# Performance work log

Hardware: AMD Instinct MI355X
Metric: run time of the kernel (lower is better)

The kernel has to match this reference:

```python
import jax, jax.numpy as jnp
import numpy as np

BSZ, SEQ, HID = 8, 4096, 1024
N_EXPERTS = 8
CAPACITY = 512  # expert_capacity_per_batch; effective cap = min(SEQ, CAPACITY)
SCALE = 1.0     # routed_scaling_factor


def setup_inputs() -> dict:
    key = jax.random.key(0)
    k1, k2 = jax.random.split(key)
    hidden_states = jax.random.normal(k1, (BSZ, SEQ, HID), dtype=jnp.float32)
    # kaiming_uniform_(a=sqrt(5)) on [d,e] -> bound = 1/sqrt(fan_in=d)
    bound = 1.0 / np.sqrt(HID)
    weight = jax.random.uniform(k2, (HID, N_EXPERTS), dtype=jnp.float32,
                                minval=-bound, maxval=bound)
    return {"hidden_states": hidden_states, "weight": weight}


def reference(hidden_states, weight):
    bsz, seq_len, h = hidden_states.shape
    # gating logits in fp32: [b, s, e]
    logits = jnp.einsum('bsd,de->bse', hidden_states.astype(jnp.float32),
                        weight.astype(jnp.float32))
    affinity = jax.nn.softmax(logits, axis=-1)          # [b, s, e]
    affinity = jnp.transpose(affinity, (0, 2, 1))       # [b, e, s]
    cap = min(seq_len, CAPACITY)                        # static
    # Each expert picks its top-`cap` tokens (sorted descending, like torch.topk)
    topk_scores, topk_indices = jax.lax.top_k(affinity, cap)  # [b, e, cap]
    topk_scores = topk_scores * SCALE
    # dense dispatch mask [b, e, cap, s]: one-hot over token positions
    dispatch_mask = jax.nn.one_hot(topk_indices, seq_len, dtype=jnp.float32)
    return topk_indices, topk_scores, dispatch_mask
```

## Files before the change

kernel.cpp:

```cpp
#include <hip/hip_runtime.h>

constexpr int BSZ = 8, SEQ = 4096, HID = 1024, NE = 8, CAP = 512;
constexpr int ROWS = BSZ * NE;
constexpr size_t IDX_ELEMS = (size_t)ROWS * CAP;
constexpr size_t SCR_OFF = IDX_ELEMS;
constexpr size_t MASK_OFF = IDX_ELEMS * 2;
constexpr size_t MASK_ELEMS = (size_t)ROWS * CAP * SEQ;
constexpr size_t AFF_ELEMS = (size_t)ROWS * SEQ;

typedef float f4v __attribute__((ext_vector_type(4)));

__global__ __launch_bounds__(128) void gating_kernel(const float* __restrict__ hidden,
                                                     const float* __restrict__ weight,
                                                     float* __restrict__ aff)
{
    __shared__ float hls[16][68];
    __shared__ float wls[8][68];
    __shared__ float lls[16][8];

    const int tid = threadIdx.x;
    const int T0 = blockIdx.x * 16;
    const int t = tid >> 3;
    const int e = tid & 7;

    float v0 = 0.f, v1 = 0.f, v2 = 0.f, v3 = 0.f;
    for (int c = 0; c < 16; ++c) {
        __syncthreads();
#pragma unroll
        for (int k = 0; k < 2; ++k) {
            const int j = tid + k * 128;
            const int tt = j >> 4, q = j & 15;
            const float4 v = *(const float4*)(hidden + (size_t)(T0 + tt) * HID + c * 64 + 4 * q);
            *(float4*)&hls[tt][4 * q] = v;
        }
#pragma unroll
        for (int k = 0; k < 4; ++k) {
            const int j = tid + k * 128;
            const int dd = j >> 3, ee = j & 7;
            wls[ee][dd] = weight[(size_t)(c * 64 + dd) * NE + ee];
        }
        __syncthreads();
#pragma unroll
        for (int k = 0; k < 4; ++k) {
            const int base = 16 * k;
            const float4 hA = *(const float4*)&hls[t][base + 0];
            const float4 hB = *(const float4*)&hls[t][base + 4];
            const float4 hC = *(const float4*)&hls[t][base + 8];
            const float4 hD = *(const float4*)&hls[t][base + 12];
            const float4 wA = *(const float4*)&wls[e][base + 0];
            const float4 wB = *(const float4*)&wls[e][base + 4];
            const float4 wC = *(const float4*)&wls[e][base + 8];
            const float4 wD = *(const float4*)&wls[e][base + 12];
            v0 = __fadd_rn(__fmul_rn(hA.x, wA.x),
                 __fadd_rn(__fmul_rn(hB.x, wB.x),
                 __fadd_rn(__fmul_rn(hC.x, wC.x),
                 __fadd_rn(__fmul_rn(hD.x, wD.x), v0))));
            v1 = __fadd_rn(__fmul_rn(hA.y, wA.y),
                 __fadd_rn(__fmul_rn(hB.y, wB.y),
                 __fadd_rn(__fmul_rn(hC.y, wC.y),
                 __fadd_rn(__fmul_rn(hD.y, wD.y), v1))));
            v2 = __fadd_rn(__fmul_rn(hA.z, wA.z),
                 __fadd_rn(__fmul_rn(hB.z, wB.z),
                 __fadd_rn(__fmul_rn(hC.z, wC.z),
                 __fadd_rn(__fmul_rn(hD.z, wD.z), v2))));
            v3 = __fadd_rn(__fmul_rn(hA.w, wA.w),
                 __fadd_rn(__fmul_rn(hB.w, wB.w),
                 __fadd_rn(__fmul_rn(hC.w, wC.w),
                 __fadd_rn(__fmul_rn(hD.w, wD.w), v3))));
        }
    }
    const float logit = __fadd_rn(__fadd_rn(v0, v1), __fadd_rn(v2, v3));

    lls[t][e] = logit;
    __syncthreads();

    float l[8];
#pragma unroll
    for (int k = 0; k < 8; ++k) l[k] = lls[t][k];
    float m = l[0];
#pragma unroll
    for (int k = 1; k < 8; ++k) m = fmaxf(m, l[k]);
    float p[8];
#pragma unroll
    for (int k = 0; k < 8; ++k)
        p[k] = (float)exp((double)__fsub_rn(l[k], m));
    const float s = __fadd_rn(__fadd_rn(__fadd_rn(p[0], p[1]), __fadd_rn(p[2], p[3])),
                              __fadd_rn(__fadd_rn(p[4], p[5]), __fadd_rn(p[6], p[7])));
    const float a = __fdiv_rn(p[e], s);

    const int token = T0 + t;
    const int b = token >> 12;
    const int sidx = token & (SEQ - 1);
    aff[((size_t)b * NE + e) * SEQ + sidx] = a;
}

__global__ __launch_bounds__(1024) void sortzero_kernel(const float* __restrict__ aff,
                                                        float* __restrict__ out)
{
    __shared__ unsigned long long keys[SEQ];
    const int row = blockIdx.x;
    const float* a = aff + (size_t)row * SEQ;
    float* mrow = out + MASK_OFF + (size_t)row * CAP * SEQ;

    for (int i = threadIdx.x; i < SEQ; i += 1024) {
        const unsigned int fb = __float_as_uint(a[i]);
        keys[i] = ((unsigned long long)fb << 32) | (unsigned int)(SEQ - 1 - i);
    }

    f4v* mz = (f4v*)mrow;
    const f4v z4 = {0.f, 0.f, 0.f, 0.f};
    int zi = 0;

    for (int len = 2; len <= SEQ; len <<= 1) {
        for (int stride = len >> 1; stride > 0; stride >>= 1) {
            __syncthreads();
#pragma unroll
            for (int k = 0; k < 7; ++k) {
                if (zi < 512) {
                    __builtin_nontemporal_store(z4, mz + (size_t)zi * 1024 + threadIdx.x);
                    ++zi;
                }
            }
            for (int t = threadIdx.x; t < SEQ / 2; t += 1024) {
                const int i = (t << 1) - (t & (stride - 1));
                const int j = i + stride;
                const unsigned long long ki = keys[i], kj = keys[j];
                const bool desc = ((i & len) == 0);
                if (desc ? (ki < kj) : (ki > kj)) { keys[i] = kj; keys[j] = ki; }
            }
        }
    }
    __syncthreads();
    if (threadIdx.x < CAP) {
        const int t = threadIdx.x;
        const unsigned long long k = keys[t];
        const int idx = (SEQ - 1) - (int)(unsigned int)(k & 0xffffffffu);
        out[(size_t)row * CAP + t] = (float)idx;
        out[SCR_OFF + (size_t)row * CAP + t] =
            __uint_as_float((unsigned int)(k >> 32));
        mrow[(size_t)t * SEQ + idx] = 1.0f;
    }
}

__global__ __launch_bounds__(1024) void topk_zero_kernel(const float* __restrict__ aff,
                                                         float* __restrict__ out,
                                                         long long zero_elems)
{
    __shared__ unsigned long long keys[SEQ];
    if (blockIdx.x < (unsigned)ROWS) {
        const int row = blockIdx.x;
        const float* a = aff + (size_t)row * SEQ;
        for (int i = threadIdx.x; i < SEQ; i += 1024) {
            const unsigned int fb = __float_as_uint(a[i]);
            keys[i] = ((unsigned long long)fb << 32) | (unsigned int)(SEQ - 1 - i);
        }
        for (int len = 2; len <= SEQ; len <<= 1) {
            for (int stride = len >> 1; stride > 0; stride >>= 1) {
                __syncthreads();
                for (int t = threadIdx.x; t < SEQ / 2; t += 1024) {
                    const int i = (t << 1) - (t & (stride - 1));
                    const int j = i + stride;
                    const unsigned long long ki = keys[i], kj = keys[j];
                    const bool desc = ((i & len) == 0);
                    if (desc ? (ki < kj) : (ki > kj)) { keys[i] = kj; keys[j] = ki; }
                }
            }
        }
        __syncthreads();
        if (threadIdx.x < CAP) {
            const int t = threadIdx.x;
            const unsigned long long k = keys[t];
            const int idx = (SEQ - 1) - (int)(unsigned int)(k & 0xffffffffu);
            out[(size_t)row * CAP + t] = (float)idx;
            out[SCR_OFF + (size_t)row * CAP + t] =
                __uint_as_float((unsigned int)(k >> 32));
        }
    } else {
        const long long nz4 = zero_elems >> 2;
        f4v* mz = (f4v*)(out + MASK_OFF);
        const f4v z4 = {0.f, 0.f, 0.f, 0.f};
        const long long stride = (long long)(gridDim.x - ROWS) * 1024;
        for (long long i = (long long)(blockIdx.x - ROWS) * 1024 + threadIdx.x;
             i < nz4; i += stride)
            __builtin_nontemporal_store(z4, mz + i);
    }
}

__global__ void tailzero_kernel(float* __restrict__ out)
{
    const long long n4 = (long long)(AFF_ELEMS >> 2);
    f4v* mz = (f4v*)(out + MASK_OFF + MASK_ELEMS - AFF_ELEMS);
    const f4v z4 = {0.f, 0.f, 0.f, 0.f};
    const long long i = (long long)blockIdx.x * blockDim.x + threadIdx.x;
    if (i < n4) __builtin_nontemporal_store(z4, mz + i);
}

__global__ void scatter_kernel(float* __restrict__ out)
{
    const int p = blockIdx.x * blockDim.x + threadIdx.x;
    if (p < (int)IDX_ELEMS) {
        const int idx = (int)out[p];
        out[MASK_OFF + (size_t)p * SEQ + idx] = 1.0f;
    }
}

extern "C" void kernel_launch(void* const* d_in, const int* in_sizes, int n_in,
                              void* d_out, int out_size, void* d_ws, size_t ws_size,
                              hipStream_t stream)
{
    const float* hidden = (const float*)d_in[0];
    const float* weight = (const float*)d_in[1];
    float* out = (float*)d_out;

    const bool use_ws = (ws_size >= AFF_ELEMS * sizeof(float));

    if (use_ws) {
        float* aff = (float*)d_ws;
        gating_kernel<<<2048, 128, 0, stream>>>(hidden, weight, aff);
        sortzero_kernel<<<ROWS, 1024, 0, stream>>>(aff, out);
    } else {
        float* aff = out + MASK_OFF + MASK_ELEMS - AFF_ELEMS;
        gating_kernel<<<2048, 128, 0, stream>>>(hidden, weight, aff);
        const long long zero_elems = (long long)(MASK_ELEMS - AFF_ELEMS);
        topk_zero_kernel<<<ROWS + 1984, 1024, 0, stream>>>(aff, out, zero_elems);
        tailzero_kernel<<<256, 256, 0, stream>>>(out);
        scatter_kernel<<<(int)((IDX_ELEMS + 255) / 256), 256, 0, stream>>>(out);
    }
}
```

Measured before the change: 640.0 us.

## Split top-k into segmented bitonic sorts plus bitonic merge-selection kernel

Replaces the one-block-per-row full 4096-element bitonic sort with a two-stage scheme. Stage one sorts each 512-element segment in 512 blocks while 1536 other blocks zero the dispatch mask. Stage two merges the segments with bitonic top-half selection and writes indices, scores and one-hot entries. The aim is more parallelism and less wasted sorting work, since only the top 512 per row are needed. It costs an extra workspace buffer for the keys, an extra global round trip and an extra launch, and it needs a larger workspace or it falls back to the old path.

```diff
diff --git a/kernel.cpp b/kernel.cpp
--- a/kernel.cpp
+++ b/kernel.cpp
@@ -7,6 +7,8 @@
 constexpr size_t MASK_OFF = IDX_ELEMS * 2;
 constexpr size_t MASK_ELEMS = (size_t)ROWS * CAP * SEQ;
 constexpr size_t AFF_ELEMS = (size_t)ROWS * SEQ;
+constexpr size_t AFF_BYTES = AFF_ELEMS * sizeof(float);
+constexpr size_t KEYS_BYTES = (size_t)ROWS * SEQ * 8;
 
 typedef float f4v __attribute__((ext_vector_type(4)));
 
@@ -94,6 +96,86 @@
     aff[((size_t)b * NE + e) * SEQ + sidx] = a;
 }
 
+__global__ __launch_bounds__(256) void segsort_zero_kernel(const float* __restrict__ aff,
+                                                           unsigned long long* __restrict__ keys,
+                                                           float* __restrict__ out)
+{
+    __shared__ unsigned long long k[512];
+    if (blockIdx.x < 512) {
+        const int row = blockIdx.x >> 3, seg = blockIdx.x & 7;
+        const int g0 = seg * 512;
+        const float* a = aff + (size_t)row * SEQ + g0;
+        for (int j = threadIdx.x; j < 512; j += 256) {
+            const unsigned int fb = __float_as_uint(a[j]);
+            k[j] = ((unsigned long long)fb << 32) | (unsigned int)(SEQ - 1 - (g0 + j));
+        }
+        for (int len = 2; len <= 512; len <<= 1) {
+            for (int stride = len >> 1; stride > 0; stride >>= 1) {
+                __syncthreads();
+                const int t = threadIdx.x;
+                const int i = (t << 1) - (t & (stride - 1));
+                const int j = i + stride;
+                const unsigned long long ki = k[i], kj = k[j];
+                const bool desc = ((i & len) == 0);
+                if (desc ? (ki < kj) : (ki > kj)) { k[i] = kj; k[j] = ki; }
+            }
+        }
+        __syncthreads();
+        unsigned long long* dst = keys + (size_t)row * SEQ + g0;
+        for (int j = threadIdx.x; j < 512; j += 256) dst[j] = k[j];
+    } else {
+        const long long nz4 = (long long)(MASK_ELEMS >> 2);
+        f4v* mz = (f4v*)(out + MASK_OFF);
+        const f4v z4 = {0.f, 0.f, 0.f, 0.f};
+        const long long stride = (long long)(2048 - 512) * 256;
+        for (long long i = (long long)(blockIdx.x - 512) * 256 + threadIdx.x;
+             i < nz4; i += stride)
+            __builtin_nontemporal_store(z4, mz + i);
+    }
+}
+
+__global__ __launch_bounds__(512) void merge_scatter_kernel(const unsigned long long* __restrict__ keys,
+                                                            float* __restrict__ out)
+{
+    __shared__ unsigned long long A[SEQ];
+    const int row = blockIdx.x;
+    for (int i = threadIdx.x; i < SEQ; i += 512)
+        A[i] = keys[(size_t)row * SEQ + i];
+
+    for (int round = 0; round < 3; ++round) {
+        const int sp = 1024 << round;
+        const int npairs = 4 >> round;
+        __syncthreads();
+        for (int u = threadIdx.x; u < npairs * 512; u += 512) {
+            const int p = u >> 9, i = u & 511;
+            const int base = p * sp;
+            const unsigned long long x = A[base + i];
+            const unsigned long long y = A[base + sp / 2 + 511 - i];
+            if (y > x) A[base + i] = y;
+        }
+        for (int s = 256; s > 0; s >>= 1) {
+            __syncthreads();
+            for (int u = threadIdx.x; u < npairs * 256; u += 512) {
+                const int r = u >> 8, t2 = u & 255;
+                const int base = r * sp;
+                const int i = (t2 << 1) - (t2 & (s - 1));
+                const unsigned long long x = A[base + i], y = A[base + i + s];
+                if (y > x) { A[base + i] = y; A[base + i + s] = x; }
+            }
+        }
+    }
+    __syncthreads();
+    if (threadIdx.x < CAP) {
+        const int t = threadIdx.x;
+        const unsigned long long k = A[t];
+        const int idx = (SEQ - 1) - (int)(unsigned int)(k & 0xffffffffu);
+        out[(size_t)row * CAP + t] = (float)idx;
+        out[SCR_OFF + (size_t)row * CAP + t] =
+            __uint_as_float((unsigned int)(k >> 32));
+        out[MASK_OFF + ((size_t)row * CAP + t) * SEQ + idx] = 1.0f;
+    }
+}
+
 __global__ __launch_bounds__(1024) void sortzero_kernel(const float* __restrict__ aff,
                                                         float* __restrict__ out)
 {
@@ -106,11 +188,9 @@
         const unsigned int fb = __float_as_uint(a[i]);
         keys[i] = ((unsigned long long)fb << 32) | (unsigned int)(SEQ - 1 - i);
     }
-
     f4v* mz = (f4v*)mrow;
     const f4v z4 = {0.f, 0.f, 0.f, 0.f};
     int zi = 0;
-
     for (int len = 2; len <= SEQ; len <<= 1) {
         for (int stride = len >> 1; stride > 0; stride >>= 1) {
             __syncthreads();
@@ -212,9 +292,13 @@
     const float* weight = (const float*)d_in[1];
     float* out = (float*)d_out;
 
-    const bool use_ws = (ws_size >= AFF_ELEMS * sizeof(float));
-
-    if (use_ws) {
+    if (ws_size >= AFF_BYTES + KEYS_BYTES) {
+        float* aff = (float*)d_ws;
+        unsigned long long* keys = (unsigned long long*)((char*)d_ws + AFF_BYTES);
+        gating_kernel<<<2048, 128, 0, stream>>>(hidden, weight, aff);
+        segsort_zero_kernel<<<2048, 256, 0, stream>>>(aff, keys, out);
+        merge_scatter_kernel<<<ROWS, 512, 0, stream>>>(keys, out);
+    } else if (ws_size >= AFF_BYTES) {
         float* aff = (float*)d_ws;
         gating_kernel<<<2048, 128, 0, stream>>>(hidden, weight, aff);
         sortzero_kernel<<<ROWS, 1024, 0, stream>>>(aff, out);
```

Result: no change. 649.0 us (+1.4%).
